# Kernel tuning notes

Hardware: AMD Instinct MI355X
Metric: run time of the kernel (lower is better)

## Reference

```python
import jax, jax.numpy as jnp
import numpy as np

N_EDGE_TYPES = 25
EF = 2  # edge feature dim (excluding type)
HID = 10


def _edge_nn(et, ef, emb, wh, bh, wg, bg):
    # y = relu(emb[et] * (ef@Wh+bh) + (ef@Wg+bg)) -> [E, in*out]
    return jax.nn.relu(emb[et] * (ef @ wh + bh) + (ef @ wg + bg))


def _nnconv(x, et, ef, src, dst, emb, wh, bh, wg, bg, root, bias, in_c, out_c):
    n = x.shape[0]
    w = _edge_nn(et, ef, emb, wh, bh, wg, bg).reshape(-1, in_c, out_c)  # [E,in,out]
    msg = jnp.einsum('ei,eio->eo', x[src], w)                          # per-edge matmul
    s = jax.ops.segment_sum(msg, dst, num_segments=n)
    cnt = jax.ops.segment_sum(jnp.ones((src.shape[0],), x.dtype), dst, num_segments=n)
    agg = s / jnp.maximum(cnt, 1.0)[:, None]                           # scatter-mean
    return agg + x @ root + bias


def _make_params(key, in_c, out_c):
    ks = jax.random.split(key, 6)
    d = in_c * out_c
    s = 0.1
    return dict(
        emb=jax.random.normal(ks[0], (N_EDGE_TYPES, d), jnp.float32) * s,
        wh=jax.random.normal(ks[1], (EF, d), jnp.float32) * s,
        bh=jax.random.normal(ks[2], (d,), jnp.float32) * s,
        wg=jax.random.normal(ks[3], (EF, d), jnp.float32) * s,
        bg=jax.random.normal(ks[4], (d,), jnp.float32) * s,
        root=jax.random.normal(ks[5], (in_c, out_c), jnp.float32) * s,
        bias=jnp.zeros((out_c,), jnp.float32),
    )


def setup_inputs() -> dict:
    key = jax.random.key(0)
    ks = jax.random.split(key, 12)
    N, E, IN_C, OUT_C, B = 50000, 250000, 16, 16, 8
    inp = {
        'x': jax.random.normal(ks[0], (N, IN_C), jnp.float32),
        'edge_feat': jax.random.normal(ks[1], (E, EF), jnp.float32),
        'edge_type': jax.random.randint(ks[2], (E,), 0, N_EDGE_TYPES),
        'edge_src': jax.random.randint(ks[3], (E,), 0, N),
        'edge_dst': jax.random.randint(ks[4], (E,), 0, N),
        'cell_type': jax.random.randint(ks[5], (N,), 0, 3),
        'batch_ids': jnp.sort(jax.random.randint(ks[6], (N,), 0, B)),
        'batch_size': B,
    }
    for i, (ic, oc) in enumerate([(IN_C, HID), (HID, HID), (HID, OUT_C)], start=1):
        p = _make_params(ks[6 + i], ic, oc)
        for k, v in p.items():
            inp[f'{k}{i}'] = v
    return inp


def reference(x, edge_feat,
              emb1, wh1, bh1, wg1, bg1, root1, bias1,
              emb2, wh2, bh2, wg2, bg2, root2, bias2,
              emb3, wh3, bh3, wg3, bg3, root3, bias3,
              edge_type, edge_src, edge_dst, cell_type, batch_ids, batch_size):
    in_c, out_c = x.shape[1], root3.shape[1]
    h = _nnconv(x, edge_type, edge_feat, edge_src, edge_dst,
                emb1, wh1, bh1, wg1, bg1, root1, bias1, in_c, HID)
    h = jax.nn.relu(h)  # dropout is identity in eval mode
    h = _nnconv(h, edge_type, edge_feat, edge_src, edge_dst,
                emb2, wh2, bh2, wg2, bg2, root2, bias2, HID, HID)
    h = jax.nn.relu(h)
    h = _nnconv(h, edge_type, edge_feat, edge_src, edge_dst,
                emb3, wh3, bh3, wg3, bg3, root3, bias3, HID, out_c)
    h = jax.nn.relu(h)
    # scatter-mean pooling over nodes with cell_type==1, grouped by graph id
    gate = (cell_type == 1).astype(jnp.int32)
    idx = gate * (batch_ids.astype(jnp.int32) + 1)  # 0 = discarded bucket
    nseg = batch_size + 1
    s = jax.ops.segment_sum(h, idx, num_segments=nseg)
    cnt = jax.ops.segment_sum(jnp.ones((h.shape[0],), h.dtype), idx, num_segments=nseg)
    pooled = s / jnp.maximum(cnt, 1.0)[:, None]
    return pooled[1:batch_size + 1, :]  # [B, out_c]
```

## Files before the change

### kernel.cpp

```cpp
#include <hip/hip_runtime.h>

#define IN1 16
#define HIDC 10
#define OUT3 16
#define NTYPES 25
#define MAXB 32

__global__ __launch_bounds__(256) void zero2_kernel(int* __restrict__ a, int na,
                                                    int* __restrict__ b, int nb) {
  int i = blockIdx.x * blockDim.x + threadIdx.x;
  int s = gridDim.x * blockDim.x;
  for (int j = i; j < na; j += s) a[j] = 0;
  for (int j = i; j < nb; j += s) b[j] = 0;
}

__global__ __launch_bounds__(256) void hist_kernel(const int* __restrict__ edst,
                                                   int* __restrict__ deg,
                                                   int* __restrict__ pos, int E) {
  int e = blockIdx.x * blockDim.x + threadIdx.x;
  if (e < E) pos[e] = atomicAdd(&deg[edst[e]], 1);
}

__global__ __launch_bounds__(1024) void scan_kernel(const int4* __restrict__ deg4,
                                                    int* __restrict__ row_ptr, int N) {
  __shared__ int wsums[16];
  __shared__ int s_run;
  int tid = threadIdx.x, lane = tid & 63, wid = tid >> 6;
  if (tid == 0) s_run = 0;
  __syncthreads();
  int N4 = (N + 3) >> 2;
  for (int base = 0; base < N4; base += 1024) {
    int i4 = base + tid;
    int4 v = make_int4(0, 0, 0, 0);
    if (i4 < N4) v = deg4[i4];
    int idx0 = i4 * 4;
    if (idx0 + 1 >= N) v.y = 0;
    if (idx0 + 2 >= N) v.z = 0;
    if (idx0 + 3 >= N) v.w = 0;
    int s = v.x + v.y + v.z + v.w;
    int x = s;
    #pragma unroll
    for (int off = 1; off < 64; off <<= 1) {
      int y = __shfl_up(x, off);
      if (lane >= off) x += y;
    }
    if (lane == 63) wsums[wid] = x;
    __syncthreads();
    if (tid < 16) {
      int w = wsums[tid];
      #pragma unroll
      for (int off = 1; off < 16; off <<= 1) {
        int y = __shfl_up(w, off);
        if (tid >= off) w += y;
      }
      wsums[tid] = w;
    }
    __syncthreads();
    int excl = x - s + ((wid > 0) ? wsums[wid - 1] : 0) + s_run;
    int total = wsums[15];
    if (idx0 < N) row_ptr[idx0] = excl;
    if (idx0 + 1 < N) row_ptr[idx0 + 1] = excl + v.x;
    if (idx0 + 2 < N) row_ptr[idx0 + 2] = excl + v.x + v.y;
    if (idx0 + 3 < N) row_ptr[idx0 + 3] = excl + v.x + v.y + v.z;
    __syncthreads();
    if (tid == 0) s_run += total;
    __syncthreads();
  }
  if (threadIdx.x == 0) row_ptr[N] = s_run;
}

__global__ __launch_bounds__(256) void permute_kernel(
    const int* __restrict__ edst, const int* __restrict__ esrc,
    const int* __restrict__ et, const float2* __restrict__ ef,
    const int* __restrict__ row_ptr, const int* __restrict__ pos,
    int4* __restrict__ edges, int E) {
  int e = blockIdx.x * blockDim.x + threadIdx.x;
  if (e >= E) return;
  int d = edst[e];
  int idx = row_ptr[d] + pos[e];
  float2 f = ef[e];
  int4 r;
  r.x = esrc[e];
  r.y = et[e];
  r.z = __float_as_int(f.x);
  r.w = __float_as_int(f.y);
  edges[idx] = r;
}

template<int IN_C, int O, bool POOL, int BS>
__global__ __launch_bounds__(BS) void layer_kernel(
    const float* __restrict__ xin,
    const int4* __restrict__ edges,
    const int* __restrict__ row_ptr,
    const float* __restrict__ emb,
    const float* __restrict__ wh, const float* __restrict__ bh,
    const float* __restrict__ wg, const float* __restrict__ bg,
    const float* __restrict__ root,
    const float* __restrict__ bias,
    float* __restrict__ hout,
    const int* __restrict__ ctype, const int* __restrict__ bids,
    float* __restrict__ pcnt,
    int N, int B)
{
  constexpr int D = IN_C * O;
  constexpr int ESTR = D + 8;
  constexpr int NPB = BS / 16;
  __shared__ float4 s_pa[D];
  __shared__ float2 s_pb[D];
  __shared__ float s_emb[NTYPES * ESTR];
  __shared__ float s_root[D];
  __shared__ float s_bias[O];
  __shared__ float s_psum[POOL ? (MAXB * 16) : 1];
  __shared__ float s_pcnt[POOL ? MAXB : 1];

  int tid = threadIdx.x;
  for (int k = tid; k < D; k += BS) {
    s_pa[k] = make_float4(wh[k], wh[D + k], wg[k], wg[D + k]);
    s_pb[k] = make_float2(bh[k], bg[k]);
    s_root[k] = root[k];
  }
  for (int k = tid; k < NTYPES * D; k += BS) {
    int t = k / D, j = k - t * D;
    s_emb[t * ESTR + j] = emb[k];
  }
  if (tid < O) s_bias[tid] = bias[tid];
  if (POOL) {
    for (int i = tid; i < MAXB * 16; i += BS) s_psum[i] = 0.f;
    for (int i = tid; i < MAXB; i += BS) s_pcnt[i] = 0.f;
  }
  __syncthreads();

  int nl = tid >> 4;
  int o = tid & 15;
  int oc = (O == 16) ? o : ((o < O) ? o : 0);
  int n = blockIdx.x * NPB + nl;

  float acc = 0.f;
  int start = 0, end = 0;
  if (n < N) { start = row_ptr[n]; end = row_ptr[n + 1]; }
  for (int e = start; e < end; ++e) {
    int4 r = edges[e];
    int src = r.x, t = r.y;
    float f0 = __int_as_float(r.z), f1 = __int_as_float(r.w);
    const float* __restrict__ xr = xin + (size_t)src * IN_C;
    const float* __restrict__ er = s_emb + t * ESTR;
    #pragma unroll
    for (int i = 0; i < IN_C; ++i) {
      int k = i * O + oc;
      float4 a = s_pa[k];
      float2 b = s_pb[k];
      float h = fmaf(f0, a.x, fmaf(f1, a.y, b.x));
      float g = fmaf(f0, a.z, fmaf(f1, a.w, b.y));
      float w = fmaxf(fmaf(er[k], h, g), 0.f);
      acc = fmaf(xr[i], w, acc);
    }
  }

  if (n < N && o < O) {
    float inv = 1.0f / fmaxf((float)(end - start), 1.0f);
    float v = fmaf(acc, inv, s_bias[o]);
    const float* __restrict__ xr = xin + (size_t)n * IN_C;
    #pragma unroll
    for (int i = 0; i < IN_C; ++i) v = fmaf(xr[i], s_root[i * O + o], v);
    v = fmaxf(v, 0.f);
    if (!POOL) {
      hout[(size_t)n * O + o] = v;
    } else {
      if (ctype[n] == 1) {
        int b = bids[n];
        atomicAdd(&s_psum[b * 16 + o], v);
        if (o == 0) atomicAdd(&s_pcnt[b], 1.0f);
      }
    }
  }

  if (POOL) {
    __syncthreads();
    for (int i = tid; i < B * 16; i += BS) {
      float v = s_psum[i];
      if (v != 0.f) atomicAdd(&hout[i], v);
    }
    for (int i = tid; i < B; i += BS) {
      float c = s_pcnt[i];
      if (c != 0.f) atomicAdd(&pcnt[i], c);
    }
  }
}

__global__ __launch_bounds__(256) void finalize_kernel(
    const float* __restrict__ psum, const float* __restrict__ pcnt,
    float* __restrict__ out, int B) {
  int i = blockIdx.x * blockDim.x + threadIdx.x;
  if (i >= B * OUT3) return;
  int b = i / OUT3;
  out[i] = psum[i] / fmaxf(pcnt[b], 1.0f);
}

extern "C" void kernel_launch(void* const* d_in, const int* in_sizes, int n_in,
                              void* d_out, int out_size, void* d_ws, size_t ws_size,
                              hipStream_t stream)
{
  const float* x     = (const float*)d_in[0];
  const float* ef    = (const float*)d_in[1];
  const int*   et    = (const int*)d_in[2];
  const int*   esrc  = (const int*)d_in[3];
  const int*   edst  = (const int*)d_in[4];
  const int*   ctype = (const int*)d_in[5];
  const int*   bids  = (const int*)d_in[6];
  const float* emb1 = (const float*)d_in[8];
  const float* wh1  = (const float*)d_in[9];
  const float* bh1  = (const float*)d_in[10];
  const float* wg1  = (const float*)d_in[11];
  const float* bg1  = (const float*)d_in[12];
  const float* root1= (const float*)d_in[13];
  const float* bias1= (const float*)d_in[14];
  const float* emb2 = (const float*)d_in[15];
  const float* wh2  = (const float*)d_in[16];
  const float* bh2  = (const float*)d_in[17];
  const float* wg2  = (const float*)d_in[18];
  const float* bg2  = (const float*)d_in[19];
  const float* root2= (const float*)d_in[20];
  const float* bias2= (const float*)d_in[21];
  const float* emb3 = (const float*)d_in[22];
  const float* wh3  = (const float*)d_in[23];
  const float* bh3  = (const float*)d_in[24];
  const float* wg3  = (const float*)d_in[25];
  const float* bg3  = (const float*)d_in[26];
  const float* root3= (const float*)d_in[27];
  const float* bias3= (const float*)d_in[28];

  const int N = in_sizes[0] / IN1;
  const int E = in_sizes[2];
  const int B = out_size / OUT3;

  int4* edges   = (int4*)d_ws;
  int*  deg     = (int*)(edges + E);
  int*  pos     = deg + N;
  int*  row_ptr = pos + E;
  float* h1     = (float*)(row_ptr + (N + 1));
  float* h2     = h1 + (size_t)N * HIDC;
  float* psum   = h2 + (size_t)N * HIDC;
  float* pcnt   = psum + (size_t)B * 16;

  zero2_kernel<<<128, 256, 0, stream>>>(deg, N, (int*)psum, B * 16 + B);
  hist_kernel<<<(E + 255) / 256, 256, 0, stream>>>(edst, deg, pos, E);
  scan_kernel<<<1, 1024, 0, stream>>>((const int4*)deg, row_ptr, N);
  permute_kernel<<<(E + 255) / 256, 256, 0, stream>>>(
      edst, esrc, et, (const float2*)ef, row_ptr, pos, edges, E);

  const int g256 = (N + 15) / 16;
  layer_kernel<IN1, HIDC, false, 256><<<g256, 256, 0, stream>>>(
      x, edges, row_ptr, emb1, wh1, bh1, wg1, bg1, root1, bias1,
      h1, nullptr, nullptr, nullptr, N, B);
  layer_kernel<HIDC, HIDC, false, 256><<<g256, 256, 0, stream>>>(
      h1, edges, row_ptr, emb2, wh2, bh2, wg2, bg2, root2, bias2,
      h2, nullptr, nullptr, nullptr, N, B);

  const int g1024 = (N + 63) / 64;
  layer_kernel<HIDC, OUT3, true, 1024><<<g1024, 1024, 0, stream>>>(
      h2, edges, row_ptr, emb3, wh3, bh3, wg3, bg3, root3, bias3,
      psum, ctype, bids, pcnt, N, B);

  finalize_kernel<<<1, 256, 0, stream>>>(psum, pcnt, (float*)d_out, B);
}
```

Before: 276.6 us.

## Pad hidden features to 16 floats and software-pipeline edge gathers with vector loads

Intermediate node features h1/h2 are stored with a stride of 16 floats in a 16-byte aligned buffer, so each source row can be fetched as float4 vector loads. The edge loop is restructured into a two-deep software pipeline that prefetches the next edge records and source rows while the current edge is computed. The dot product also uses two accumulators to shorten the FMA dependency chain. This trades extra register pressure and a larger workspace for hiding gather latency. With HID=10, each padded row reads 12 floats instead of 10.

```diff
diff --git a/kernel.cpp b/kernel.cpp
--- a/kernel.cpp
+++ b/kernel.cpp
@@ -1,10 +1,12 @@
 #include <hip/hip_runtime.h>
+#include <stdint.h>
 
 #define IN1 16
 #define HIDC 10
 #define OUT3 16
 #define NTYPES 25
 #define MAXB 32
+#define XSTR 16
 
 __global__ __launch_bounds__(256) void zero2_kernel(int* __restrict__ a, int na,
                                                     int* __restrict__ b, int nb) {
@@ -105,6 +107,7 @@
   constexpr int D = IN_C * O;
   constexpr int ESTR = D + 8;
   constexpr int NPB = BS / 16;
+  constexpr int XQ = (IN_C + 3) / 4;
   __shared__ float4 s_pa[D];
   __shared__ float2 s_pb[D];
   __shared__ float s_emb[NTYPES * ESTR];
@@ -135,14 +138,27 @@
   int oc = (O == 16) ? o : ((o < O) ? o : 0);
   int n = blockIdx.x * NPB + nl;
 
-  float acc = 0.f;
+  float acc0 = 0.f, acc1 = 0.f;
   int start = 0, end = 0;
   if (n < N) { start = row_ptr[n]; end = row_ptr[n + 1]; }
-  for (int e = start; e < end; ++e) {
-    int4 r = edges[e];
-    int src = r.x, t = r.y;
+  int nE = end - start;
+  const int4* __restrict__ ep = edges + start;
+
+  float xa[4 * XQ], xb[4 * XQ];
+  int4 rA = make_int4(0, 0, 0, 0), rB = make_int4(0, 0, 0, 0);
+
+  auto loadx = [&](float* xd, int src) {
+    const float4* __restrict__ p = (const float4*)(xin + (size_t)src * XSTR);
+    #pragma unroll
+    for (int q = 0; q < XQ; ++q) {
+      float4 v = p[q];
+      xd[4 * q + 0] = v.x; xd[4 * q + 1] = v.y;
+      xd[4 * q + 2] = v.z; xd[4 * q + 3] = v.w;
+    }
+  };
+  auto edge_compute = [&](const int4& r, const float* xd) {
+    int t = r.y;
     float f0 = __int_as_float(r.z), f1 = __int_as_float(r.w);
-    const float* __restrict__ xr = xin + (size_t)src * IN_C;
     const float* __restrict__ er = s_emb + t * ESTR;
     #pragma unroll
     for (int i = 0; i < IN_C; ++i) {
@@ -152,19 +168,48 @@
       float h = fmaf(f0, a.x, fmaf(f1, a.y, b.x));
       float g = fmaf(f0, a.z, fmaf(f1, a.w, b.y));
       float w = fmaxf(fmaf(er[k], h, g), 0.f);
-      acc = fmaf(xr[i], w, acc);
-    }
-  }
+      if (i & 1) acc1 = fmaf(xd[i], w, acc1);
+      else       acc0 = fmaf(xd[i], w, acc0);
+    }
+  };
+
+  if (nE > 0) {
+    rA = ep[0];
+    if (nE > 1) rB = ep[1];
+    loadx(xa, rA.x);
+    if (nE > 1) loadx(xb, rB.x);
+    int j = 0;
+    while (true) {
+      {
+        bool pf = (j + 2 < nE);
+        int4 rn = make_int4(0, 0, 0, 0);
+        if (pf) rn = ep[j + 2];
+        edge_compute(rA, xa);
+        if (pf) { rA = rn; loadx(xa, rA.x); }
+      }
+      if (++j >= nE) break;
+      {
+        bool pf = (j + 2 < nE);
+        int4 rn = make_int4(0, 0, 0, 0);
+        if (pf) rn = ep[j + 2];
+        edge_compute(rB, xb);
+        if (pf) { rB = rn; loadx(xb, rB.x); }
+      }
+      if (++j >= nE) break;
+    }
+  }
+
+  float acc = acc0 + acc1;
 
   if (n < N && o < O) {
-    float inv = 1.0f / fmaxf((float)(end - start), 1.0f);
+    float inv = 1.0f / fmaxf((float)nE, 1.0f);
     float v = fmaf(acc, inv, s_bias[o]);
-    const float* __restrict__ xr = xin + (size_t)n * IN_C;
+    const float* __restrict__ xr = xin + (size_t)n * XSTR;
     #pragma unroll
     for (int i = 0; i < IN_C; ++i) v = fmaf(xr[i], s_root[i * O + o], v);
     v = fmaxf(v, 0.f);
     if (!POOL) {
-      hout[(size_t)n * O + o] = v;
+      hout[(size_t)n * XSTR + o] = v;
     } else {
       if (ctype[n] == 1) {
         int b = bids[n];
@@ -237,9 +282,9 @@
   int*  deg     = (int*)(edges + E);
   int*  pos     = deg + N;
   int*  row_ptr = pos + E;
-  float* h1     = (float*)(row_ptr + (N + 1));
-  float* h2     = h1 + (size_t)N * HIDC;
-  float* psum   = h2 + (size_t)N * HIDC;
+  float* h1 = (float*)((((uintptr_t)(row_ptr + (N + 1))) + 15) & ~(uintptr_t)15);
+  float* h2     = h1 + (size_t)N * XSTR;
+  float* psum   = h2 + (size_t)N * XSTR;
   float* pcnt   = psum + (size_t)B * 16;
 
   zero2_kernel<<<128, 256, 0, stream>>>(deg, N, (int*)psum, B * 16 + B);
```

Result: slower. 299.0 us (+8.1%).

## Replace single-block prefix scan with three-pass multi-block scan

Applied to the files above, without the earlier changes.

The degree prefix scan used to run in one 1024-thread block that looped serially over all N nodes. It now runs as three kernels: a per-chunk scan across about 49 blocks, a one-wave scan of the chunk totals, and an add pass that applies the chunk offsets. This spreads the scan across many compute units instead of one, at the cost of two extra launches and an extra read and write of row_ptr. The chunk-total scan holds at most 64 chunks, so it only covers N up to 65536.

```diff
diff --git a/kernel.cpp b/kernel.cpp
--- a/kernel.cpp
+++ b/kernel.cpp
@@ -1,4 +1,5 @@
 #include <hip/hip_runtime.h>
+#include <stdint.h>
 
 #define IN1 16
 #define HIDC 10
@@ -21,52 +22,57 @@
   if (e < E) pos[e] = atomicAdd(&deg[edst[e]], 1);
 }
 
-__global__ __launch_bounds__(1024) void scan_kernel(const int4* __restrict__ deg4,
-                                                    int* __restrict__ row_ptr, int N) {
-  __shared__ int wsums[16];
-  __shared__ int s_run;
+__global__ __launch_bounds__(256) void scan_part_kernel(const int* __restrict__ deg,
+                                                        int* __restrict__ row_ptr,
+                                                        int* __restrict__ bsum, int N) {
+  __shared__ int wsums[4];
   int tid = threadIdx.x, lane = tid & 63, wid = tid >> 6;
-  if (tid == 0) s_run = 0;
+  int idx0 = (blockIdx.x * 256 + tid) * 4;
+  int4 v = make_int4(0, 0, 0, 0);
+  if (idx0 < N)     v.x = deg[idx0];
+  if (idx0 + 1 < N) v.y = deg[idx0 + 1];
+  if (idx0 + 2 < N) v.z = deg[idx0 + 2];
+  if (idx0 + 3 < N) v.w = deg[idx0 + 3];
+  int s = v.x + v.y + v.z + v.w;
+  int x = s;
+  #pragma unroll
+  for (int off = 1; off < 64; off <<= 1) {
+    int y = __shfl_up(x, off);
+    if (lane >= off) x += y;
+  }
+  if (lane == 63) wsums[wid] = x;
   __syncthreads();
-  int N4 = (N + 3) >> 2;
-  for (int base = 0; base < N4; base += 1024) {
-    int i4 = base + tid;
-    int4 v = make_int4(0, 0, 0, 0);
-    if (i4 < N4) v = deg4[i4];
-    int idx0 = i4 * 4;
-    if (idx0 + 1 >= N) v.y = 0;
-    if (idx0 + 2 >= N) v.z = 0;
-    if (idx0 + 3 >= N) v.w = 0;
-    int s = v.x + v.y + v.z + v.w;
-    int x = s;
-    #pragma unroll
-    for (int off = 1; off < 64; off <<= 1) {
-      int y = __shfl_up(x, off);
-      if (lane >= off) x += y;
-    }
-    if (lane == 63) wsums[wid] = x;
-    __syncthreads();
-    if (tid < 16) {
-      int w = wsums[tid];
-      #pragma unroll
-      for (int off = 1; off < 16; off <<= 1) {
-        int y = __shfl_up(w, off);
-        if (tid >= off) w += y;
-      }
-      wsums[tid] = w;
-    }
-    __syncthreads();
-    int excl = x - s + ((wid > 0) ? wsums[wid - 1] : 0) + s_run;
-    int total = wsums[15];
-    if (idx0 < N) row_ptr[idx0] = excl;
-    if (idx0 + 1 < N) row_ptr[idx0 + 1] = excl + v.x;
-    if (idx0 + 2 < N) row_ptr[idx0 + 2] = excl + v.x + v.y;
-    if (idx0 + 3 < N) row_ptr[idx0 + 3] = excl + v.x + v.y + v.z;
-    __syncthreads();
-    if (tid == 0) s_run += total;
-    __syncthreads();
-  }
-  if (threadIdx.x == 0) row_ptr[N] = s_run;
+  int wpre = 0;
+  #pragma unroll
+  for (int w = 0; w < 4; ++w) if (w < wid) wpre += wsums[w];
+  int excl = x - s + wpre;
+  if (idx0 < N)     row_ptr[idx0]     = excl;
+  if (idx0 + 1 < N) row_ptr[idx0 + 1] = excl + v.x;
+  if (idx0 + 2 < N) row_ptr[idx0 + 2] = excl + v.x + v.y;
+  if (idx0 + 3 < N) row_ptr[idx0 + 3] = excl + v.x + v.y + v.z;
+  if (tid == 255) bsum[blockIdx.x] = excl + s;
+}
+
+__global__ __launch_bounds__(64) void scan_bsum_kernel(int* __restrict__ bsum,
+                                                       int* __restrict__ row_ptr,
+                                                       int G, int N) {
+  int tid = threadIdx.x;
+  int v = (tid < G) ? bsum[tid] : 0;
+  int x = v;
+  #pragma unroll
+  for (int off = 1; off < 64; off <<= 1) {
+    int y = __shfl_up(x, off);
+    if (tid >= off) x += y;
+  }
+  if (tid < G) bsum[tid] = x - v;
+  if (tid == 63) row_ptr[N] = x;
+}
+
+__global__ __launch_bounds__(256) void scan_add_kernel(int* __restrict__ row_ptr,
+                                                       const int* __restrict__ bsum,
+                                                       int N) {
+  int i = blockIdx.x * blockDim.x + threadIdx.x;
+  if (i < N) row_ptr[i] += bsum[i >> 10];
 }
 
 __global__ __launch_bounds__(256) void permute_kernel(
@@ -237,14 +243,19 @@
   int*  deg     = (int*)(edges + E);
   int*  pos     = deg + N;
   int*  row_ptr = pos + E;
-  float* h1     = (float*)(row_ptr + (N + 1));
+  int*  bsum    = row_ptr + (N + 1);
+  float* h1     = (float*)(bsum + 64);
   float* h2     = h1 + (size_t)N * HIDC;
   float* psum   = h2 + (size_t)N * HIDC;
   float* pcnt   = psum + (size_t)B * 16;
 
+  const int nChunk = (N + 1023) / 1024;
+
   zero2_kernel<<<128, 256, 0, stream>>>(deg, N, (int*)psum, B * 16 + B);
   hist_kernel<<<(E + 255) / 256, 256, 0, stream>>>(edst, deg, pos, E);
-  scan_kernel<<<1, 1024, 0, stream>>>((const int4*)deg, row_ptr, N);
+  scan_part_kernel<<<nChunk, 256, 0, stream>>>(deg, row_ptr, bsum, N);
+  scan_bsum_kernel<<<1, 64, 0, stream>>>(bsum, row_ptr, nChunk, N);
+  scan_add_kernel<<<(N + 255) / 256, 256, 0, stream>>>(row_ptr, bsum, N);
   permute_kernel<<<(E + 255) / 256, 256, 0, stream>>>(
       edst, esrc, et, (const float2*)ef, row_ptr, pos, edges, E);
 
```

Result: faster. 257.9 us (-6.8%).
